# Optimization experiments

Hardware: AMD Instinct MI355X
Metric: run time of the kernel (lower is better)

## Reference

```python
import jax, jax.numpy as jnp
import numpy as np

B, HID, NUM_RIS = 65536, 256, 64
R = NUM_RIS // 4  # number of 4-qubit circuit runs


def _cnot_perm(c, t):
    # basis index i has wire 0 as most-significant bit (matches shape (2,2,2,2) row-major)
    idx = np.arange(16)
    cbit = (idx >> (3 - c)) & 1
    return idx ^ (cbit << (3 - t))

P01 = jnp.asarray(_cnot_perm(0, 1))
P23 = jnp.asarray(_cnot_perm(2, 3))
P12 = jnp.asarray(_cnot_perm(1, 2))
P30 = jnp.asarray(_cnot_perm(3, 0))


def apply_ry(state, theta, wire):
    # state: (B, R, 2,2,2,2); theta broadcastable to (B, R)
    ax = 2 + wire
    c = jnp.cos(theta * 0.5)[..., None, None, None]
    s = jnp.sin(theta * 0.5)[..., None, None, None]
    s0 = jnp.take(state, 0, axis=ax)
    s1 = jnp.take(state, 1, axis=ax)
    return jnp.stack([c * s0 - s * s1, s * s0 + c * s1], axis=ax)


def apply_cnot(state, perm):
    b, r = state.shape[:2]
    return state.reshape(b, r, 16)[:, :, perm].reshape(b, r, 2, 2, 2, 2)


def setup_inputs() -> dict:
    key = jax.random.key(0)
    k1, k2, k3 = jax.random.split(key, 3)
    fused = jax.random.normal(k1, (B, HID), dtype=jnp.float32)
    W_proj = jax.random.normal(k2, (4 * R, HID), dtype=jnp.float32) * (1.0 / np.sqrt(HID))
    b_proj = jnp.zeros((4 * R,), dtype=jnp.float32)
    vqc_weights = jax.random.normal(k3, (R, 4, 4), dtype=jnp.float32) * 0.01
    return {"fused": fused, "W_proj": W_proj, "b_proj": b_proj, "vqc_weights": vqc_weights}


def reference(fused, W_proj, b_proj, vqc_weights):
    b = fused.shape[0]
    r = vqc_weights.shape[0]
    angles = jnp.tanh(fused @ W_proj.T + b_proj) * jnp.pi  # (B, 4R)
    angles = angles.reshape(b, r, 4)

    # initial |0000> state, batched over (B, R)
    state = jnp.zeros((b, r, 2, 2, 2, 2), dtype=fused.dtype).at[:, :, 0, 0, 0, 0].set(1.0)

    # input encoding layer
    for w in range(4):
        state = apply_ry(state, angles[:, :, w], w)
    # variational layer 0 + entanglers
    for w in range(4):
        state = apply_ry(state, vqc_weights[:, 0, w][None], w)
    state = apply_cnot(state, P01)
    state = apply_cnot(state, P23)
    # layer 1
    for w in range(4):
        state = apply_ry(state, vqc_weights[:, 1, w][None], w)
    state = apply_cnot(state, P12)
    state = apply_cnot(state, P30)
    # layer 2
    for w in range(4):
        state = apply_ry(state, vqc_weights[:, 2, w][None], w)
    state = apply_cnot(state, P01)
    state = apply_cnot(state, P12)
    state = apply_cnot(state, P23)
    state = apply_cnot(state, P30)
    # layer 3
    for w in range(4):
        state = apply_ry(state, vqc_weights[:, 3, w][None], w)

    # <Z_w> = sum(p | bit_w=0) - sum(p | bit_w=1)
    prob = state * state  # RY/CNOT keep state real
    evs = []
    for w in range(4):
        ax = 2 + w
        diff = jnp.take(prob, 0, axis=ax) - jnp.take(prob, 1, axis=ax)
        evs.append(diff.sum(axis=(2, 3, 4)))  # (B, R)
    z = jnp.stack(evs, axis=-1).reshape(b, r * 4)  # matches torch.cat over runs
    return (z + 1.0) * jnp.pi
```

## Files before the change

### kernel.cpp

```cpp
#include <hip/hip_runtime.h>
#include <math.h>


#define PI_F 3.14159265358979323846f

typedef _Float16 f16x4 __attribute__((ext_vector_type(4)));
typedef _Float16 f16x8 __attribute__((ext_vector_type(8)));
typedef float    f32x4 __attribute__((ext_vector_type(4)));
typedef float    f32x16 __attribute__((ext_vector_type(16)));

__device__ __forceinline__ void ry_gate(float st[16], float c, float s, int w) {
    const int m = 1 << (3 - w);
    #pragma unroll
    for (int i = 0; i < 16; ++i) {
        if (i & m) continue;
        float a = st[i];
        float b = st[i | m];
        st[i]     = c * a - s * b;
        st[i | m] = s * a + c * b;
    }
}

__device__ __forceinline__ void cnot_gate(float st[16], int cw, int tw) {
    const int cm = 1 << (3 - cw);
    const int tm = 1 << (3 - tw);
    #pragma unroll
    for (int i = 0; i < 16; ++i) {
        if ((i & cm) && !(i & tm)) {
            float tmp = st[i];
            st[i] = st[i | tm];
            st[i | tm] = tmp;
        }
    }
}

__global__ void prep_kernel(const float* __restrict__ vw,
                            const float* __restrict__ W,
                            char* __restrict__ ws) {
    const int tid = threadIdx.x;
    if (blockIdx.x == 0) {
        float* Ut = (float*)(ws + 49152);
        {
            const int r = tid >> 4, j = tid & 15;
            const float* wr = vw + r * 16;
            float cs[16], sn[16];
            #pragma unroll
            for (int i = 0; i < 16; ++i) {
                float h = wr[i] * 0.5f;
                cs[i] = __cosf(h);
                sn[i] = __sinf(h);
            }
            float st[16];
            #pragma unroll
            for (int i = 0; i < 16; ++i) st[i] = 0.f;
            st[j] = 1.f;
            #pragma unroll
            for (int w = 0; w < 4; ++w) ry_gate(st, cs[w], sn[w], w);
            cnot_gate(st, 0, 1);
            cnot_gate(st, 2, 3);
            #pragma unroll
            for (int w = 0; w < 4; ++w) ry_gate(st, cs[4 + w], sn[4 + w], w);
            cnot_gate(st, 1, 2);
            cnot_gate(st, 3, 0);
            #pragma unroll
            for (int w = 0; w < 4; ++w) ry_gate(st, cs[8 + w], sn[8 + w], w);
            cnot_gate(st, 0, 1);
            cnot_gate(st, 1, 2);
            cnot_gate(st, 2, 3);
            cnot_gate(st, 3, 0);
            #pragma unroll
            for (int w = 0; w < 4; ++w) ry_gate(st, cs[12 + w], sn[12 + w], w);
            #pragma unroll
            for (int i = 0; i < 16; ++i) Ut[r * 256 + i * 16 + j] = st[i];
        }
        __syncthreads();
        {
            _Float16* UA = (_Float16*)(ws + 32768);
            #pragma unroll
            for (int t = 0; t < 4; ++t) {
                int f = t * 256 + tid;
                int r = f >> 6, lane = f & 63;
                int i = lane & 31, hh = lane >> 5;
                const float* urow = Ut + r * 256 + (i & 15) * 16;
                f16x8 h;
                #pragma unroll
                for (int e = 0; e < 8; ++e) {
                    float u = urow[8 * hh + e];
                    if (i < 16) {
                        h[e] = (_Float16)u;
                    } else {
                        _Float16 hi = (_Float16)u;
                        h[e] = (_Float16)(u - (float)hi);
                    }
                }
                *(f16x8*)(UA + f * 8) = h;
            }
        }
    } else {
        _Float16* Wh = (_Float16*)ws;
        #pragma unroll
        for (int t = 0; t < 8; ++t) {
            int f  = tid * 8 + t;
            int cg = f >> 9;
            int kk = (f >> 6) & 7;
            int l  = f & 63;
            int row = cg * 16 + (l & 15);
            int k0  = (kk * 4 + (l >> 4)) * 8;
            const float* src = W + row * 256 + k0;
            f16x8 h;
            #pragma unroll
            for (int e = 0; e < 8; ++e) h[e] = (_Float16)src[e];
            *(f16x8*)(Wh + f * 8) = h;
        }
    }
}

#define NT 2

__global__ __launch_bounds__(256, 3) void vqc_main_kernel(
        const float* __restrict__ fused,
        const char* __restrict__ ws,
        const float* __restrict__ bp,
        float* __restrict__ out) {
    __shared__ __align__(16) char smem[16384 + 16 * 32 * 16];

    const int tid  = threadIdx.x;
    const int lane = tid & 63;
    const int cg   = tid >> 6;
    const int l15  = lane & 15;
    const int l4   = lane >> 4;

    float4 stg[8];
    {
        const float4* s4 = (const float4*)(fused + (size_t)blockIdx.x * NT * 8192);
        #pragma unroll
        for (int it = 0; it < 8; ++it) stg[it] = s4[tid + it * 256];
    }

    const f16x8* Wf = (const f16x8*)ws;
    f16x8 af[8];
    #pragma unroll
    for (int kk = 0; kk < 8; ++kk) af[kk] = Wf[(cg * 8 + kk) * 64 + lane];

    const f16x8* UA = (const f16x8*)(ws + 32768);
    f16x8 ua[4];
    #pragma unroll
    for (int rr = 0; rr < 4; ++rr) ua[rr] = UA[(4 * cg + rr) * 64 + lane];

    float4 bb = *(const float4*)(bp + 4 * (4 * cg + l4));

    _Float16* tab = (_Float16*)(smem + 16384);
    const int r_own = 4 * cg + l4;
    const int s32   = lane & 31;
    const int hh    = lane >> 5;
    const float g1  = hh ? -1.f : 1.f;

    #pragma unroll 1
    for (int t = 0; t < NT; ++t) {
        const size_t tb = (size_t)blockIdx.x * NT + t;
        const size_t b0 = tb * 32;

        if (t > 0) __syncthreads();

        #pragma unroll
        for (int it = 0; it < 8; ++it) {
            int q = tid + it * 256;
            float4 v = stg[it];
            int row = q >> 6;
            int c4  = (q & 63) << 2;
            int sl  = (c4 >> 3) ^ (row & 7);
            int byteoff = row * 512 + (sl << 4) + ((c4 & 7) << 1);
            f16x4 h = { (_Float16)v.x, (_Float16)v.y, (_Float16)v.z, (_Float16)v.w };
            *(f16x4*)(smem + byteoff) = h;
        }

        if (t + 1 < NT) {
            const float4* s4 = (const float4*)(fused + (tb + 1) * 8192);
            #pragma unroll
            for (int it = 0; it < 8; ++it) stg[it] = s4[tid + it * 256];
        }

        __syncthreads();

        f32x4 acc[2] = {};
        #pragma unroll
        for (int kk = 0; kk < 8; ++kk) {
            int slot = kk * 4 + l4;
            #pragma unroll
            for (int sg = 0; sg < 2; ++sg) {
                int frow = sg * 16 + l15;
                f16x8 bf = *(const f16x8*)(smem + frow * 512 + ((slot ^ (frow & 7)) << 4));
                acc[sg] = __builtin_amdgcn_mfma_f32_16x16x32_f16(af[kk], bf, acc[sg], 0, 0, 0);
            }
        }

        #pragma unroll
        for (int sg = 0; sg < 2; ++sg) {
            float bias[4] = {bb.x, bb.y, bb.z, bb.w};
            float cc[4], ssn[4];
            #pragma unroll
            for (int w = 0; w < 4; ++w) {
                float pre = acc[sg][w] + bias[w];
                float e   = __expf(2.f * pre);
                float th  = __fdividef(e - 1.f, e + 1.f);
                float ha  = th * (0.5f * PI_F);
                __sincosf(ha, &ssn[w], &cc[w]);
            }
            f16x8 tt;
            tt[0] = (_Float16)(cc[0] * cc[1]);  tt[1] = (_Float16)(cc[0] * ssn[1]);
            tt[2] = (_Float16)(ssn[0] * cc[1]); tt[3] = (_Float16)(ssn[0] * ssn[1]);
            tt[4] = (_Float16)(cc[2] * cc[3]);  tt[5] = (_Float16)(cc[2] * ssn[3]);
            tt[6] = (_Float16)(ssn[2] * cc[3]); tt[7] = (_Float16)(ssn[2] * ssn[3]);
            *(f16x8*)(tab + (r_own * 32 + sg * 16 + l15) * 8) = tt;
        }

        #pragma unroll
        for (int rr = 0; rr < 4; ++rr) {
            const int r = 4 * cg + rr;
            f16x8 tt = *(const f16x8*)(tab + (r * 32 + s32) * 8);
            _Float16 a0 = tt[2 * hh], a1 = tt[2 * hh + 1];
            f16x8 se;
            se[0] = a0 * tt[4]; se[1] = a0 * tt[5];
            se[2] = a0 * tt[6]; se[3] = a0 * tt[7];
            se[4] = a1 * tt[4]; se[5] = a1 * tt[5];
            se[6] = a1 * tt[6]; se[7] = a1 * tt[7];

            f32x16 zero = {};
            f32x16 o = __builtin_amdgcn_mfma_f32_32x32x16_f16(ua[rr], se, zero, 0, 0, 0);

            float p[8];
            #pragma unroll
            for (int j = 0; j < 8; ++j) {
                float of = o[j] + o[j + 8];
                p[j] = of * of;
            }
            float a = p[0] + p[1], b = p[2] + p[3];
            float c = p[4] + p[5], d = p[6] + p[7];
            float ab = a + b, cd = c + d;
            float z0 = ab - cd;
            float z1 = g1 * (ab + cd);
            float z2 = (a - b) + (c - d);
            float z3 = (p[0] - p[1] + p[2] - p[3]) + (p[4] - p[5] + p[6] - p[7]);

            z0 += __shfl_xor(z0, 32);
            z1 += __shfl_xor(z1, 32);
            z2 += __shfl_xor(z2, 32);
            z3 += __shfl_xor(z3, 32);

            if (hh == 0) {
                float4 ov;
                ov.x = (z0 + 1.f) * PI_F;
                ov.y = (z1 + 1.f) * PI_F;
                ov.z = (z2 + 1.f) * PI_F;
                ov.w = (z3 + 1.f) * PI_F;
                *(float4*)(out + (b0 + s32) * 64 + 4 * r) = ov;
            }
        }
    }
}

extern "C" void kernel_launch(void* const* d_in, const int* in_sizes, int n_in,
                              void* d_out, int out_size, void* d_ws, size_t ws_size,
                              hipStream_t stream) {
    const float* fused = (const float*)d_in[0];
    const float* Wp    = (const float*)d_in[1];
    const float* bp    = (const float*)d_in[2];
    const float* vw    = (const float*)d_in[3];
    float* out = (float*)d_out;
    char*  ws  = (char*)d_ws;

    prep_kernel<<<2, 256, 0, stream>>>(vw, Wp, ws);

    const int B = 65536;
    vqc_main_kernel<<<B / (32 * NT), 256, 0, stream>>>(fused, ws, bp, out);
}
```

Before: 28.85 us.

## Fuse weight-prep into main kernel, recomputing circuit unitary per block

Removes the separate prep kernel launch by having every block build the fixed 16x16 circuit unitary (split into hi/lo fp16 parts) and convert W to fp16 MFMA fragments itself, staging through shared memory. The per-block tile loop is dropped: each block now handles 32 rows, the grid doubles, and the occupancy hint rises from 3 to 4. The bias is folded into the accumulator's initial value. This saves a launch and the dependency between the two kernels, but every block now repeats the unitary simulation and reads and converts W from fp32, and it loses the prefetch overlap of the old two-tile loop.

After: 32.01 us. 1.11x slower.

```diff
diff --git a/kernel.cpp b/kernel.cpp
--- a/kernel.cpp
+++ b/kernel.cpp
@@ -34,227 +34,220 @@
     }
 }
 
-__global__ void prep_kernel(const float* __restrict__ vw,
-                            const float* __restrict__ W,
-                            char* __restrict__ ws) {
-    const int tid = threadIdx.x;
-    if (blockIdx.x == 0) {
-        float* Ut = (float*)(ws + 49152);
-        {
-            const int r = tid >> 4, j = tid & 15;
-            const float* wr = vw + r * 16;
-            float cs[16], sn[16];
-            #pragma unroll
-            for (int i = 0; i < 16; ++i) {
-                float h = wr[i] * 0.5f;
-                cs[i] = __cosf(h);
-                sn[i] = __sinf(h);
-            }
-            float st[16];
-            #pragma unroll
-            for (int i = 0; i < 16; ++i) st[i] = 0.f;
-            st[j] = 1.f;
-            #pragma unroll
-            for (int w = 0; w < 4; ++w) ry_gate(st, cs[w], sn[w], w);
-            cnot_gate(st, 0, 1);
-            cnot_gate(st, 2, 3);
-            #pragma unroll
-            for (int w = 0; w < 4; ++w) ry_gate(st, cs[4 + w], sn[4 + w], w);
-            cnot_gate(st, 1, 2);
-            cnot_gate(st, 3, 0);
-            #pragma unroll
-            for (int w = 0; w < 4; ++w) ry_gate(st, cs[8 + w], sn[8 + w], w);
-            cnot_gate(st, 0, 1);
-            cnot_gate(st, 1, 2);
-            cnot_gate(st, 2, 3);
-            cnot_gate(st, 3, 0);
-            #pragma unroll
-            for (int w = 0; w < 4; ++w) ry_gate(st, cs[12 + w], sn[12 + w], w);
-            #pragma unroll
-            for (int i = 0; i < 16; ++i) Ut[r * 256 + i * 16 + j] = st[i];
-        }
-        __syncthreads();
-        {
-            _Float16* UA = (_Float16*)(ws + 32768);
-            #pragma unroll
-            for (int t = 0; t < 4; ++t) {
-                int f = t * 256 + tid;
-                int r = f >> 6, lane = f & 63;
-                int i = lane & 31, hh = lane >> 5;
-                const float* urow = Ut + r * 256 + (i & 15) * 16;
-                f16x8 h;
-                #pragma unroll
-                for (int e = 0; e < 8; ++e) {
-                    float u = urow[8 * hh + e];
-                    if (i < 16) {
-                        h[e] = (_Float16)u;
-                    } else {
-                        _Float16 hi = (_Float16)u;
-                        h[e] = (_Float16)(u - (float)hi);
-                    }
-                }
-                *(f16x8*)(UA + f * 8) = h;
-            }
-        }
-    } else {
-        _Float16* Wh = (_Float16*)ws;
-        #pragma unroll
-        for (int t = 0; t < 8; ++t) {
-            int f  = tid * 8 + t;
-            int cg = f >> 9;
-            int kk = (f >> 6) & 7;
-            int l  = f & 63;
-            int row = cg * 16 + (l & 15);
-            int k0  = (kk * 4 + (l >> 4)) * 8;
-            const float* src = W + row * 256 + k0;
-            f16x8 h;
-            #pragma unroll
-            for (int e = 0; e < 8; ++e) h[e] = (_Float16)src[e];
-            *(f16x8*)(Wh + f * 8) = h;
-        }
-    }
-}
-
-#define NT 2
-
-__global__ __launch_bounds__(256, 3) void vqc_main_kernel(
+__global__ __launch_bounds__(256, 4) void vqc_fused_kernel(
         const float* __restrict__ fused,
-        const char* __restrict__ ws,
+        const float* __restrict__ W,
         const float* __restrict__ bp,
+        const float* __restrict__ vw,
         float* __restrict__ out) {
-    __shared__ __align__(16) char smem[16384 + 16 * 32 * 16];
+    __shared__ __align__(16) char smem[28672];
+    float*    Ucols = (float*)smem;
+    _Float16* tab   = (_Float16*)(smem + 20480);
 
     const int tid  = threadIdx.x;
     const int lane = tid & 63;
     const int cg   = tid >> 6;
     const int l15  = lane & 15;
     const int l4   = lane >> 4;
+    const size_t b0 = (size_t)blockIdx.x * 32;
 
     float4 stg[8];
     {
-        const float4* s4 = (const float4*)(fused + (size_t)blockIdx.x * NT * 8192);
+        const float4* s4 = (const float4*)(fused + b0 * 256);
         #pragma unroll
         for (int it = 0; it < 8; ++it) stg[it] = s4[tid + it * 256];
     }
 
-    const f16x8* Wf = (const f16x8*)ws;
+    const int r_own = 4 * cg + l4;
+    const float* vwr = vw + r_own * 16;
+    float st[16];
+    {
+        float4 th = *(const float4*)vwr;
+        float c, s;
+        float f0a, f0b, f1a, f1b, f2a, f2b, f3a, f3b;
+        __sincosf(th.x * 0.5f, &s, &c);
+        if ((l15 >> 3) & 1) { f0a = -s; f0b = c; } else { f0a = c; f0b = s; }
+        __sincosf(th.y * 0.5f, &s, &c);
+        if ((l15 >> 2) & 1) { f1a = -s; f1b = c; } else { f1a = c; f1b = s; }
+        __sincosf(th.z * 0.5f, &s, &c);
+        if ((l15 >> 1) & 1) { f2a = -s; f2b = c; } else { f2a = c; f2b = s; }
+        __sincosf(th.w * 0.5f, &s, &c);
+        if (l15 & 1)        { f3a = -s; f3b = c; } else { f3a = c; f3b = s; }
+        float a01[4] = {f0a * f1a, f0a * f1b, f0b * f1a, f0b * f1b};
+        float a23[4] = {f2a * f3a, f2a * f3b, f2b * f3a, f2b * f3b};
+        #pragma unroll
+        for (int hi = 0; hi < 4; ++hi)
+            #pragma unroll
+            for (int lo = 0; lo < 4; ++lo)
+                st[hi * 4 + lo] = a01[hi] * a23[lo];
+    }
+    cnot_gate(st, 0, 1);
+    cnot_gate(st, 2, 3);
+    {
+        float4 th = *(const float4*)(vwr + 4);
+        float c, s;
+        __sincosf(th.x * 0.5f, &s, &c); ry_gate(st, c, s, 0);
+        __sincosf(th.y * 0.5f, &s, &c); ry_gate(st, c, s, 1);
+        __sincosf(th.z * 0.5f, &s, &c); ry_gate(st, c, s, 2);
+        __sincosf(th.w * 0.5f, &s, &c); ry_gate(st, c, s, 3);
+    }
+    cnot_gate(st, 1, 2);
+    cnot_gate(st, 3, 0);
+    {
+        float4 th = *(const float4*)(vwr + 8);
+        float c, s;
+        __sincosf(th.x * 0.5f, &s, &c); ry_gate(st, c, s, 0);
+        __sincosf(th.y * 0.5f, &s, &c); ry_gate(st, c, s, 1);
+        __sincosf(th.z * 0.5f, &s, &c); ry_gate(st, c, s, 2);
+        __sincosf(th.w * 0.5f, &s, &c); ry_gate(st, c, s, 3);
+    }
+    cnot_gate(st, 0, 1);
+    cnot_gate(st, 1, 2);
+    cnot_gate(st, 2, 3);
+    cnot_gate(st, 3, 0);
+    {
+        float4 th = *(const float4*)(vwr + 12);
+        float c, s;
+        __sincosf(th.x * 0.5f, &s, &c); ry_gate(st, c, s, 0);
+        __sincosf(th.y * 0.5f, &s, &c); ry_gate(st, c, s, 1);
+        __sincosf(th.z * 0.5f, &s, &c); ry_gate(st, c, s, 2);
+        __sincosf(th.w * 0.5f, &s, &c); ry_gate(st, c, s, 3);
+    }
+
+    {
+        float* myU = Ucols + cg * 1280 + l4 * 320;
+        #pragma unroll
+        for (int i = 0; i < 16; ++i) myU[i * 20 + l15] = st[i];
+    }
+    f16x8 ua[4];
+    {
+        const int selo = (lane >> 4) & 1;
+        const int hbit = lane >> 5;
+        #pragma unroll
+        for (int rr = 0; rr < 4; ++rr) {
+            const float* up = Ucols + cg * 1280 + rr * 320 + l15 * 20 + 8 * hbit;
+            float4 u0 = *(const float4*)up;
+            float4 u1 = *(const float4*)(up + 4);
+            float uu[8] = {u0.x, u0.y, u0.z, u0.w, u1.x, u1.y, u1.z, u1.w};
+            #pragma unroll
+            for (int e = 0; e < 8; ++e) {
+                _Float16 hi = (_Float16)uu[e];
+                _Float16 lo = (_Float16)(uu[e] - (float)hi);
+                ua[rr][e] = selo ? lo : hi;
+            }
+        }
+    }
+
     f16x8 af[8];
-    #pragma unroll
-    for (int kk = 0; kk < 8; ++kk) af[kk] = Wf[(cg * 8 + kk) * 64 + lane];
-
-    const f16x8* UA = (const f16x8*)(ws + 32768);
-    f16x8 ua[4];
-    #pragma unroll
-    for (int rr = 0; rr < 4; ++rr) ua[rr] = UA[(4 * cg + rr) * 64 + lane];
-
-    float4 bb = *(const float4*)(bp + 4 * (4 * cg + l4));
-
-    _Float16* tab = (_Float16*)(smem + 16384);
-    const int r_own = 4 * cg + l4;
-    const int s32   = lane & 31;
-    const int hh    = lane >> 5;
+    {
+        const float* Wr = W + (size_t)(cg * 16 + l15) * 256;
+        #pragma unroll
+        for (int kk = 0; kk < 8; ++kk) {
+            const float* wp = Wr + (kk * 4 + l4) * 8;
+            float4 w0 = *(const float4*)wp;
+            float4 w1 = *(const float4*)(wp + 4);
+            f16x8 h;
+            h[0] = (_Float16)w0.x; h[1] = (_Float16)w0.y;
+            h[2] = (_Float16)w0.z; h[3] = (_Float16)w0.w;
+            h[4] = (_Float16)w1.x; h[5] = (_Float16)w1.y;
+            h[6] = (_Float16)w1.z; h[7] = (_Float16)w1.w;
+            af[kk] = h;
+        }
+    }
+    float4 bb = *(const float4*)(bp + 4 * r_own);
+
+    __syncthreads();
+
+    #pragma unroll
+    for (int it = 0; it < 8; ++it) {
+        int q = tid + it * 256;
+        float4 v = stg[it];
+        int row = q >> 6;
+        int c4  = (q & 63) << 2;
+        int sl  = (c4 >> 3) ^ (row & 7);
+        int byteoff = row * 512 + (sl << 4) + ((c4 & 7) << 1);
+        f16x4 h = { (_Float16)v.x, (_Float16)v.y, (_Float16)v.z, (_Float16)v.w };
+        *(f16x4*)(smem + byteoff) = h;
+    }
+    __syncthreads();
+
+    f32x4 acc[2];
+    acc[0][0] = bb.x; acc[0][1] = bb.y; acc[0][2] = bb.z; acc[0][3] = bb.w;
+    acc[1] = acc[0];
+    #pragma unroll
+    for (int kk = 0; kk < 8; ++kk) {
+        int slot = kk * 4 + l4;
+        #pragma unroll
+        for (int sg = 0; sg < 2; ++sg) {
+            int frow = sg * 16 + l15;
+            f16x8 bf = *(const f16x8*)(smem + frow * 512 + ((slot ^ (frow & 7)) << 4));
+            acc[sg] = __builtin_amdgcn_mfma_f32_16x16x32_f16(af[kk], bf, acc[sg], 0, 0, 0);
+        }
+    }
+
+    #pragma unroll
+    for (int sg = 0; sg < 2; ++sg) {
+        float cc[4], ssn[4];
+        #pragma unroll
+        for (int w = 0; w < 4; ++w) {
+            float pre = acc[sg][w];
+            float e   = __expf(2.f * pre);
+            float th  = __fdividef(e - 1.f, e + 1.f);
+            float ha  = th * (0.5f * PI_F);
+            __sincosf(ha, &ssn[w], &cc[w]);
+        }
+        f16x8 tt;
+        tt[0] = (_Float16)(cc[0] * cc[1]);  tt[1] = (_Float16)(cc[0] * ssn[1]);
+        tt[2] = (_Float16)(ssn[0] * cc[1]); tt[3] = (_Float16)(ssn[0] * ssn[1]);
+        tt[4] = (_Float16)(cc[2] * cc[3]);  tt[5] = (_Float16)(cc[2] * ssn[3]);
+        tt[6] = (_Float16)(ssn[2] * cc[3]); tt[7] = (_Float16)(ssn[2] * ssn[3]);
+        *(f16x8*)(tab + (r_own * 32 + sg * 16 + l15) * 8) = tt;
+    }
+
+    const int   s32 = lane & 31;
+    const int   hh  = lane >> 5;
     const float g1  = hh ? -1.f : 1.f;
 
-    #pragma unroll 1
-    for (int t = 0; t < NT; ++t) {
-        const size_t tb = (size_t)blockIdx.x * NT + t;
-        const size_t b0 = tb * 32;
-
-        if (t > 0) __syncthreads();
-
-        #pragma unroll
-        for (int it = 0; it < 8; ++it) {
-            int q = tid + it * 256;
-            float4 v = stg[it];
-            int row = q >> 6;
-            int c4  = (q & 63) << 2;
-            int sl  = (c4 >> 3) ^ (row & 7);
-            int byteoff = row * 512 + (sl << 4) + ((c4 & 7) << 1);
-            f16x4 h = { (_Float16)v.x, (_Float16)v.y, (_Float16)v.z, (_Float16)v.w };
-            *(f16x4*)(smem + byteoff) = h;
-        }
-
-        if (t + 1 < NT) {
-            const float4* s4 = (const float4*)(fused + (tb + 1) * 8192);
-            #pragma unroll
-            for (int it = 0; it < 8; ++it) stg[it] = s4[tid + it * 256];
-        }
-
-        __syncthreads();
-
-        f32x4 acc[2] = {};
-        #pragma unroll
-        for (int kk = 0; kk < 8; ++kk) {
-            int slot = kk * 4 + l4;
-            #pragma unroll
-            for (int sg = 0; sg < 2; ++sg) {
-                int frow = sg * 16 + l15;
-                f16x8 bf = *(const f16x8*)(smem + frow * 512 + ((slot ^ (frow & 7)) << 4));
-                acc[sg] = __builtin_amdgcn_mfma_f32_16x16x32_f16(af[kk], bf, acc[sg], 0, 0, 0);
-            }
-        }
-
-        #pragma unroll
-        for (int sg = 0; sg < 2; ++sg) {
-            float bias[4] = {bb.x, bb.y, bb.z, bb.w};
-            float cc[4], ssn[4];
-            #pragma unroll
-            for (int w = 0; w < 4; ++w) {
-                float pre = acc[sg][w] + bias[w];
-                float e   = __expf(2.f * pre);
-                float th  = __fdividef(e - 1.f, e + 1.f);
-                float ha  = th * (0.5f * PI_F);
-                __sincosf(ha, &ssn[w], &cc[w]);
-            }
-            f16x8 tt;
-            tt[0] = (_Float16)(cc[0] * cc[1]);  tt[1] = (_Float16)(cc[0] * ssn[1]);
-            tt[2] = (_Float16)(ssn[0] * cc[1]); tt[3] = (_Float16)(ssn[0] * ssn[1]);
-            tt[4] = (_Float16)(cc[2] * cc[3]);  tt[5] = (_Float16)(cc[2] * ssn[3]);
-            tt[6] = (_Float16)(ssn[2] * cc[3]); tt[7] = (_Float16)(ssn[2] * ssn[3]);
-            *(f16x8*)(tab + (r_own * 32 + sg * 16 + l15) * 8) = tt;
-        }
-
-        #pragma unroll
-        for (int rr = 0; rr < 4; ++rr) {
-            const int r = 4 * cg + rr;
-            f16x8 tt = *(const f16x8*)(tab + (r * 32 + s32) * 8);
-            _Float16 a0 = tt[2 * hh], a1 = tt[2 * hh + 1];
-            f16x8 se;
-            se[0] = a0 * tt[4]; se[1] = a0 * tt[5];
-            se[2] = a0 * tt[6]; se[3] = a0 * tt[7];
-            se[4] = a1 * tt[4]; se[5] = a1 * tt[5];
-            se[6] = a1 * tt[6]; se[7] = a1 * tt[7];
-
-            f32x16 zero = {};
-            f32x16 o = __builtin_amdgcn_mfma_f32_32x32x16_f16(ua[rr], se, zero, 0, 0, 0);
-
-            float p[8];
-            #pragma unroll
-            for (int j = 0; j < 8; ++j) {
-                float of = o[j] + o[j + 8];
-                p[j] = of * of;
-            }
-            float a = p[0] + p[1], b = p[2] + p[3];
-            float c = p[4] + p[5], d = p[6] + p[7];
-            float ab = a + b, cd = c + d;
-            float z0 = ab - cd;
-            float z1 = g1 * (ab + cd);
-            float z2 = (a - b) + (c - d);
-            float z3 = (p[0] - p[1] + p[2] - p[3]) + (p[4] - p[5] + p[6] - p[7]);
-
-            z0 += __shfl_xor(z0, 32);
-            z1 += __shfl_xor(z1, 32);
-            z2 += __shfl_xor(z2, 32);
-            z3 += __shfl_xor(z3, 32);
-
-            if (hh == 0) {
-                float4 ov;
-                ov.x = (z0 + 1.f) * PI_F;
-                ov.y = (z1 + 1.f) * PI_F;
-                ov.z = (z2 + 1.f) * PI_F;
-                ov.w = (z3 + 1.f) * PI_F;
-                *(float4*)(out + (b0 + s32) * 64 + 4 * r) = ov;
-            }
+    #pragma unroll
+    for (int rr = 0; rr < 4; ++rr) {
+        const int r = 4 * cg + rr;
+        f16x8 tt = *(const f16x8*)(tab + (r * 32 + s32) * 8);
+        _Float16 a0 = tt[2 * hh], a1 = tt[2 * hh + 1];
+        f16x8 se;
+        se[0] = a0 * tt[4]; se[1] = a0 * tt[5];
+        se[2] = a0 * tt[6]; se[3] = a0 * tt[7];
+        se[4] = a1 * tt[4]; se[5] = a1 * tt[5];
+        se[6] = a1 * tt[6]; se[7] = a1 * tt[7];
+
+        f32x16 zero = {};
+        f32x16 o = __builtin_amdgcn_mfma_f32_32x32x16_f16(ua[rr], se, zero, 0, 0, 0);
+
+        float p[8];
+        #pragma unroll
+        for (int j = 0; j < 8; ++j) {
+            float of = o[j] + o[j + 8];
+            p[j] = of * of;
+        }
+        float a = p[0] + p[1], b = p[2] + p[3];
+        float c = p[4] + p[5], d = p[6] + p[7];
+        float ab = a + b, cd = c + d;
+        float z0 = ab - cd;
+        float z1 = g1 * (ab + cd);
+        float z2 = (a - b) + (c - d);
+        float z3 = (p[0] - p[1] + p[2] - p[3]) + (p[4] - p[5] + p[6] - p[7]);
+
+        z0 += __shfl_xor(z0, 32);
+        z1 += __shfl_xor(z1, 32);
+        z2 += __shfl_xor(z2, 32);
+        z3 += __shfl_xor(z3, 32);
+
+        if (hh == 0) {
+            float4 ov;
+            ov.x = (z0 + 1.f) * PI_F;
+            ov.y = (z1 + 1.f) * PI_F;
+            ov.z = (z2 + 1.f) * PI_F;
+            ov.w = (z3 + 1.f) * PI_F;
+            *(float4*)(out + (b0 + s32) * 64 + 4 * r) = ov;
         }
     }
 }
@@ -267,10 +260,7 @@
     const float* bp    = (const float*)d_in[2];
     const float* vw    = (const float*)d_in[3];
     float* out = (float*)d_out;
-    char*  ws  = (char*)d_ws;
-
-    prep_kernel<<<2, 256, 0, stream>>>(vw, Wp, ws);
 
     const int B = 65536;
-    vqc_main_kernel<<<B / (32 * NT), 256, 0, stream>>>(fused, ws, bp, out);
-}
+    vqc_fused_kernel<<<B / 32, 256, 0, stream>>>(fused, Wp, bp, vw, out);
+}
```

## Process one 32-row tile per block and raise occupancy to 8 blocks/CU

Applied to the files above, without the earlier changes.

Drops the two-tile software-pipelined loop so each block handles a single 32-row batch tile, doubling the grid. Weight fragments are now loaded inside the MFMA loop rather than held in registers for the whole kernel. The angle table reuses the staging shared memory after a barrier, which shrinks LDS to 16 KB. Launch bounds are raised from 3 to 8 to allow more resident waves. The aim is to hide latency through occupancy instead of the manual prefetch, at the cost of reloading W and U fragments in every block and losing the overlap of the next tile's global load.

Result: no change. 28.92 us (+0.3%).

```diff
diff --git a/kernel.cpp b/kernel.cpp
--- a/kernel.cpp
+++ b/kernel.cpp
@@ -115,85 +115,59 @@
     }
 }
 
-#define NT 2
-
-__global__ __launch_bounds__(256, 3) void vqc_main_kernel(
+__global__ __launch_bounds__(256, 8) void vqc_main_kernel(
         const float* __restrict__ fused,
         const char* __restrict__ ws,
         const float* __restrict__ bp,
         float* __restrict__ out) {
-    __shared__ __align__(16) char smem[16384 + 16 * 32 * 16];
+    __shared__ __align__(16) char smem[16384];
+    _Float16* tab = (_Float16*)smem;
 
     const int tid  = threadIdx.x;
     const int lane = tid & 63;
     const int cg   = tid >> 6;
     const int l15  = lane & 15;
     const int l4   = lane >> 4;
+    const size_t b0 = (size_t)blockIdx.x * 32;
 
     float4 stg[8];
     {
-        const float4* s4 = (const float4*)(fused + (size_t)blockIdx.x * NT * 8192);
+        const float4* s4 = (const float4*)(fused + b0 * 256);
         #pragma unroll
         for (int it = 0; it < 8; ++it) stg[it] = s4[tid + it * 256];
     }
 
+    #pragma unroll
+    for (int it = 0; it < 8; ++it) {
+        int q = tid + it * 256;
+        float4 v = stg[it];
+        int row = q >> 6;
+        int c4  = (q & 63) << 2;
+        int sl  = (c4 >> 3) ^ (row & 7);
+        int byteoff = row * 512 + (sl << 4) + ((c4 & 7) << 1);
+        f16x4 h = { (_Float16)v.x, (_Float16)v.y, (_Float16)v.z, (_Float16)v.w };
+        *(f16x4*)(smem + byteoff) = h;
+    }
+    __syncthreads();
+
     const f16x8* Wf = (const f16x8*)ws;
-    f16x8 af[8];
-    #pragma unroll
-    for (int kk = 0; kk < 8; ++kk) af[kk] = Wf[(cg * 8 + kk) * 64 + lane];
-
-    const f16x8* UA = (const f16x8*)(ws + 32768);
-    f16x8 ua[4];
-    #pragma unroll
-    for (int rr = 0; rr < 4; ++rr) ua[rr] = UA[(4 * cg + rr) * 64 + lane];
-
-    float4 bb = *(const float4*)(bp + 4 * (4 * cg + l4));
-
-    _Float16* tab = (_Float16*)(smem + 16384);
+    f32x4 acc[2] = {};
+    #pragma unroll
+    for (int kk = 0; kk < 8; ++kk) {
+        f16x8 af = Wf[(cg * 8 + kk) * 64 + lane];
+        int slot = kk * 4 + l4;
+        #pragma unroll
+        for (int sg = 0; sg < 2; ++sg) {
+            int frow = sg * 16 + l15;
+            f16x8 bf = *(const f16x8*)(smem + frow * 512 + ((slot ^ (frow & 7)) << 4));
+            acc[sg] = __builtin_amdgcn_mfma_f32_16x16x32_f16(af, bf, acc[sg], 0, 0, 0);
+        }
+    }
+    __syncthreads();
+
     const int r_own = 4 * cg + l4;
-    const int s32   = lane & 31;
-    const int hh    = lane >> 5;
-    const float g1  = hh ? -1.f : 1.f;
-
-    #pragma unroll 1
-    for (int t = 0; t < NT; ++t) {
-        const size_t tb = (size_t)blockIdx.x * NT + t;
-        const size_t b0 = tb * 32;
-
-        if (t > 0) __syncthreads();
-
-        #pragma unroll
-        for (int it = 0; it < 8; ++it) {
-            int q = tid + it * 256;
-            float4 v = stg[it];
-            int row = q >> 6;
-            int c4  = (q & 63) << 2;
-            int sl  = (c4 >> 3) ^ (row & 7);
-            int byteoff = row * 512 + (sl << 4) + ((c4 & 7) << 1);
-            f16x4 h = { (_Float16)v.x, (_Float16)v.y, (_Float16)v.z, (_Float16)v.w };
-            *(f16x4*)(smem + byteoff) = h;
-        }
-
-        if (t + 1 < NT) {
-            const float4* s4 = (const float4*)(fused + (tb + 1) * 8192);
-            #pragma unroll
-            for (int it = 0; it < 8; ++it) stg[it] = s4[tid + it * 256];
-        }
-
-        __syncthreads();
-
-        f32x4 acc[2] = {};
-        #pragma unroll
-        for (int kk = 0; kk < 8; ++kk) {
-            int slot = kk * 4 + l4;
-            #pragma unroll
-            for (int sg = 0; sg < 2; ++sg) {
-                int frow = sg * 16 + l15;
-                f16x8 bf = *(const f16x8*)(smem + frow * 512 + ((slot ^ (frow & 7)) << 4));
-                acc[sg] = __builtin_amdgcn_mfma_f32_16x16x32_f16(af[kk], bf, acc[sg], 0, 0, 0);
-            }
-        }
-
+    {
+        float4 bb = *(const float4*)(bp + 4 * r_own);
         #pragma unroll
         for (int sg = 0; sg < 2; ++sg) {
             float bias[4] = {bb.x, bb.y, bb.z, bb.w};
@@ -213,48 +187,54 @@
             tt[6] = (_Float16)(ssn[2] * cc[3]); tt[7] = (_Float16)(ssn[2] * ssn[3]);
             *(f16x8*)(tab + (r_own * 32 + sg * 16 + l15) * 8) = tt;
         }
-
-        #pragma unroll
-        for (int rr = 0; rr < 4; ++rr) {
-            const int r = 4 * cg + rr;
-            f16x8 tt = *(const f16x8*)(tab + (r * 32 + s32) * 8);
-            _Float16 a0 = tt[2 * hh], a1 = tt[2 * hh + 1];
-            f16x8 se;
-            se[0] = a0 * tt[4]; se[1] = a0 * tt[5];
-            se[2] = a0 * tt[6]; se[3] = a0 * tt[7];
-            se[4] = a1 * tt[4]; se[5] = a1 * tt[5];
-            se[6] = a1 * tt[6]; se[7] = a1 * tt[7];
-
-            f32x16 zero = {};
-            f32x16 o = __builtin_amdgcn_mfma_f32_32x32x16_f16(ua[rr], se, zero, 0, 0, 0);
-
-            float p[8];
-            #pragma unroll
-            for (int j = 0; j < 8; ++j) {
-                float of = o[j] + o[j + 8];
-                p[j] = of * of;
-            }
-            float a = p[0] + p[1], b = p[2] + p[3];
-            float c = p[4] + p[5], d = p[6] + p[7];
-            float ab = a + b, cd = c + d;
-            float z0 = ab - cd;
-            float z1 = g1 * (ab + cd);
-            float z2 = (a - b) + (c - d);
-            float z3 = (p[0] - p[1] + p[2] - p[3]) + (p[4] - p[5] + p[6] - p[7]);
-
-            z0 += __shfl_xor(z0, 32);
-            z1 += __shfl_xor(z1, 32);
-            z2 += __shfl_xor(z2, 32);
-            z3 += __shfl_xor(z3, 32);
-
-            if (hh == 0) {
-                float4 ov;
-                ov.x = (z0 + 1.f) * PI_F;
-                ov.y = (z1 + 1.f) * PI_F;
-                ov.z = (z2 + 1.f) * PI_F;
-                ov.w = (z3 + 1.f) * PI_F;
-                *(float4*)(out + (b0 + s32) * 64 + 4 * r) = ov;
-            }
+    }
+
+    const f16x8* UA = (const f16x8*)(ws + 32768);
+    const int   s32 = lane & 31;
+    const int   hh  = lane >> 5;
+    const float g1  = hh ? -1.f : 1.f;
+
+    #pragma unroll
+    for (int rr = 0; rr < 4; ++rr) {
+        const int r = 4 * cg + rr;
+        f16x8 ua = UA[r * 64 + lane];
+        f16x8 tt = *(const f16x8*)(tab + (r * 32 + s32) * 8);
+        _Float16 a0 = tt[2 * hh], a1 = tt[2 * hh + 1];
+        f16x8 se;
+        se[0] = a0 * tt[4]; se[1] = a0 * tt[5];
+        se[2] = a0 * tt[6]; se[3] = a0 * tt[7];
+        se[4] = a1 * tt[4]; se[5] = a1 * tt[5];
+        se[6] = a1 * tt[6]; se[7] = a1 * tt[7];
+
+        f32x16 zero = {};
+        f32x16 o = __builtin_amdgcn_mfma_f32_32x32x16_f16(ua, se, zero, 0, 0, 0);
+
+        float p[8];
+        #pragma unroll
+        for (int j = 0; j < 8; ++j) {
+            float of = o[j] + o[j + 8];
+            p[j] = of * of;
+        }
+        float a = p[0] + p[1], b = p[2] + p[3];
+        float c = p[4] + p[5], d = p[6] + p[7];
+        float ab = a + b, cd = c + d;
+        float z0 = ab - cd;
+        float z1 = g1 * (ab + cd);
+        float z2 = (a - b) + (c - d);
+        float z3 = (p[0] - p[1] + p[2] - p[3]) + (p[4] - p[5] + p[6] - p[7]);
+
+        z0 += __shfl_xor(z0, 32);
+        z1 += __shfl_xor(z1, 32);
+        z2 += __shfl_xor(z2, 32);
+        z3 += __shfl_xor(z3, 32);
+
+        if (hh == 0) {
+            float4 ov;
+            ov.x = (z0 + 1.f) * PI_F;
+            ov.y = (z1 + 1.f) * PI_F;
+            ov.z = (z2 + 1.f) * PI_F;
+            ov.w = (z3 + 1.f) * PI_F;
+            *(float4*)(out + (b0 + s32) * 64 + 4 * r) = ov;
         }
     }
 }
@@ -272,5 +252,5 @@
     prep_kernel<<<2, 256, 0, stream>>>(vw, Wp, ws);
 
     const int B = 65536;
-    vqc_main_kernel<<<B / (32 * NT), 256, 0, stream>>>(fused, ws, bp, out);
-}
+    vqc_main_kernel<<<B / 32, 256, 0, stream>>>(fused, ws, bp, out);
+}
```
